# Kernel tuning notes

Hardware: AMD Instinct MI355X
Metric: run time of the kernel (lower is better)

The kernel has to match this reference:

```python
import jax, jax.numpy as jnp
import numpy as np

N_HEAD = 16
D_MODEL = 1024
D_HEAD = D_MODEL // N_HEAD  # 64
B, S = 1, 4096


def setup_inputs() -> dict:
    key = jax.random.key(0)
    ks = jax.random.split(key, 7)
    q = jax.random.normal(ks[0], (B, S, D_MODEL), dtype=jnp.float32)
    k = jax.random.normal(ks[1], (B, S, D_MODEL), dtype=jnp.float32)
    v = jax.random.normal(ks[2], (B, S, D_MODEL), dtype=jnp.float32)
    mask = jnp.ones((S, S), dtype=bool)
    # params match torch.rand init (uniform [0,1)); use uniform here too
    w_q = jax.random.uniform(ks[3], (D_MODEL, D_MODEL), dtype=jnp.float32)
    w_k = jax.random.uniform(ks[4], (D_HEAD, D_MODEL), dtype=jnp.float32)
    w_v = jax.random.uniform(ks[5], (D_HEAD, D_MODEL), dtype=jnp.float32)
    w_out = jax.random.uniform(ks[6], (D_MODEL, D_MODEL), dtype=jnp.float32)
    return {"q": q, "k": k, "v": v, "mask": mask,
            "w_q": w_q, "w_k": w_k, "w_v": w_v, "w_out": w_out}


def reference(q, k, v, mask, w_q, w_k, w_v, w_out):
    # F.linear(x, W) == x @ W.T
    query = q @ w_q.T                      # [b, n, d_model]
    key = k @ w_k.T                        # [b, s, d_head]  (single shared KV head)
    value = v @ w_v.T                      # [b, s, d_head]
    b, n, _ = query.shape
    query = query.reshape(b, n, N_HEAD, D_HEAD).transpose(0, 2, 1, 3)  # b h n d
    scores = jnp.einsum('bhnd,bsd->bhns', query, key) / jnp.sqrt(jnp.float32(D_HEAD))
    scores = jnp.where(mask[None, None], scores, jnp.float32(-jnp.inf))
    attn = jax.nn.softmax(scores, axis=-1)             # [b, h, n, s]
    out = jnp.einsum('bhns,bsd->bhnd', attn, value)    # [b, h, n, d]
    out = out.transpose(0, 2, 1, 3).reshape(b, n, D_MODEL)
    return out @ w_out.T
```

## Files before the change

kernel.cpp:

```cpp
#include <hip/hip_runtime.h>
#include <cstdint>
#include <cstddef>

#define S_LEN   4096
#define DM      1024
#define NHEAD   16
#define DH      64

typedef short bf16x8 __attribute__((ext_vector_type(8)));
typedef _Float16 f16x8 __attribute__((ext_vector_type(8)));
typedef float f32x4  __attribute__((ext_vector_type(4)));

__device__ __forceinline__ unsigned short f2bf(float x) {
    uint32_t u = __float_as_uint(x);
    u += 0x7fffu + ((u >> 16) & 1u);
    return (unsigned short)(u >> 16);
}
__device__ __forceinline__ float bf2f(unsigned short u) {
    return __uint_as_float(((uint32_t)u) << 16);
}
__device__ __forceinline__ unsigned pack_bf2(float a, float b) {
    return (unsigned)f2bf(a) | ((unsigned)f2bf(b) << 16);
}
__device__ __forceinline__ unsigned short f2h(float x) {
    _Float16 h = (_Float16)x;
    return __builtin_bit_cast(unsigned short, h);
}
__device__ __forceinline__ unsigned pack_h2(float a, float b) {
    return __builtin_bit_cast(unsigned, __builtin_amdgcn_cvt_pkrtz(a, b));
}
__device__ __forceinline__ void gl_lds16(const unsigned short* g, unsigned short* l) {
    __builtin_amdgcn_global_load_lds(
        (const __attribute__((address_space(1))) unsigned int*)g,
        (__attribute__((address_space(3))) unsigned int*)l, 16, 0, 0);
}
__device__ __forceinline__ void split8(const float4& a0, const float4& a1,
                                       ushort4& h0, ushort4& h1,
                                       ushort4& l0, ushort4& l1) {
    h0.x = f2bf(a0.x); l0.x = f2bf(a0.x - bf2f(h0.x));
    h0.y = f2bf(a0.y); l0.y = f2bf(a0.y - bf2f(h0.y));
    h0.z = f2bf(a0.z); l0.z = f2bf(a0.z - bf2f(h0.z));
    h0.w = f2bf(a0.w); l0.w = f2bf(a0.w - bf2f(h0.w));
    h1.x = f2bf(a1.x); l1.x = f2bf(a1.x - bf2f(h1.x));
    h1.y = f2bf(a1.y); l1.y = f2bf(a1.y - bf2f(h1.y));
    h1.z = f2bf(a1.z); l1.z = f2bf(a1.z - bf2f(h1.z));
    h1.w = f2bf(a1.w); l1.w = f2bf(a1.w - bf2f(h1.w));
}

__global__ void cvt_qw(const float* __restrict__ q, const float* __restrict__ wq,
                       const float* __restrict__ wo,
                       unsigned short* __restrict__ qh, unsigned short* __restrict__ ql,
                       unsigned short* __restrict__ wqh, unsigned short* __restrict__ wql,
                       unsigned short* __restrict__ woh)
{
    const int G1 = 1048576, GW = 262144;
    int i = blockIdx.x * blockDim.x + threadIdx.x;
    const float* src; unsigned short* h; unsigned short* l = nullptr; int off;
    if (i < G1)            { src = q;  h = qh;  l = ql;  off = i; }
    else if (i < G1 + GW)  { src = wq; h = wqh; l = wql; off = i - G1; }
    else                   { src = wo; h = woh;          off = i - G1 - GW; }
    float4 vv = reinterpret_cast<const float4*>(src)[off];
    ushort4 hh;
    hh.x = f2bf(vv.x); hh.y = f2bf(vv.y); hh.z = f2bf(vv.z); hh.w = f2bf(vv.w);
    reinterpret_cast<ushort4*>(h)[off] = hh;
    if (l) {
        ushort4 ll;
        ll.x = f2bf(vv.x - bf2f(hh.x)); ll.y = f2bf(vv.y - bf2f(hh.y));
        ll.z = f2bf(vv.z - bf2f(hh.z)); ll.w = f2bf(vv.w - bf2f(hh.w));
        reinterpret_cast<ushort4*>(l)[off] = ll;
    }
}

__launch_bounds__(256)
__global__ void kv_proj(const float* __restrict__ kin, const float* __restrict__ vin,
                        const float* __restrict__ wk, const float* __restrict__ wv,
                        unsigned short* __restrict__ Kf, unsigned short* __restrict__ Vtf)
{
    __shared__ unsigned short As_h[64][72];
    __shared__ unsigned short Bs_h[64][72];
    __shared__ unsigned short As_l[64][72];
    __shared__ unsigned short Bs_l[64][72];

    const int tid  = threadIdx.x;
    const int wave = tid >> 6;
    const int lane = tid & 63;
    const int lm   = lane & 15;
    const int quad = lane >> 4;
    const int m0   = blockIdx.x * 64;
    const bool isK = (blockIdx.y == 0);
    const float* A = isK ? kin : vin;
    const float* B = isK ? wk : wv;

    f32x4 acc[4] = {};

    for (int kc = 0; kc < DM; kc += 64) {
        __syncthreads();
#pragma unroll
        for (int i = 0; i < 2; ++i) {
            int c   = tid + i * 256;
            int r   = c >> 3;
            int col = (c & 7) * 8;
            float4 a0 = *(const float4*)&A[(size_t)(m0 + r) * DM + kc + col];
            float4 a1 = *(const float4*)&A[(size_t)(m0 + r) * DM + kc + col + 4];
            float4 b0 = *(const float4*)&B[(size_t)r * DM + kc + col];
            float4 b1 = *(const float4*)&B[(size_t)r * DM + kc + col + 4];
            ushort4 h0, h1, l0, l1;
            split8(a0, a1, h0, h1, l0, l1);
            *(ushort4*)&As_h[r][col] = h0;  *(ushort4*)&As_h[r][col + 4] = h1;
            if (isK) { *(ushort4*)&As_l[r][col] = l0;  *(ushort4*)&As_l[r][col + 4] = l1; }
            split8(b0, b1, h0, h1, l0, l1);
            *(ushort4*)&Bs_h[r][col] = h0;  *(ushort4*)&Bs_h[r][col + 4] = h1;
            if (isK) { *(ushort4*)&Bs_l[r][col] = l0;  *(ushort4*)&Bs_l[r][col + 4] = l1; }
        }
        __syncthreads();
#pragma unroll
        for (int kk = 0; kk < 64; kk += 32) {
            bf16x8 bh = *(const bf16x8*)&Bs_h[wave * 16 + lm][kk + quad * 8];
            bf16x8 bl;
            if (isK) bl = *(const bf16x8*)&Bs_l[wave * 16 + lm][kk + quad * 8];
#pragma unroll
            for (int ms = 0; ms < 4; ++ms) {
                bf16x8 ah = *(const bf16x8*)&As_h[ms * 16 + lm][kk + quad * 8];
                acc[ms] = __builtin_amdgcn_mfma_f32_16x16x32_bf16(ah, bh, acc[ms], 0, 0, 0);
                if (isK) {
                    bf16x8 al = *(const bf16x8*)&As_l[ms * 16 + lm][kk + quad * 8];
                    acc[ms] = __builtin_amdgcn_mfma_f32_16x16x32_bf16(ah, bl, acc[ms], 0, 0, 0);
                    acc[ms] = __builtin_amdgcn_mfma_f32_16x16x32_bf16(al, bh, acc[ms], 0, 0, 0);
                }
            }
        }
    }

#pragma unroll
    for (int ms = 0; ms < 4; ++ms)
#pragma unroll
        for (int r = 0; r < 4; ++r) {
            int row = m0 + ms * 16 + quad * 4 + r;
            int col = wave * 16 + lm;
            if (isK) Kf[(size_t)row * DH + col] = f2h(acc[ms][r]);
            else     Vtf[(size_t)col * S_LEN + row] = f2h(acc[ms][r]);
        }
}

__launch_bounds__(256)
__global__ void gemm_big(const unsigned short* __restrict__ Ah,
                         const unsigned short* __restrict__ Al,
                         const unsigned short* __restrict__ Bh,
                         const unsigned short* __restrict__ Bl,
                         unsigned short* __restrict__ Ch,
                         int M, int N, int K, int ldc)
{
    __shared__ unsigned short As_h[2][8192];
    __shared__ unsigned short Bs_h[2][8192];
    __shared__ unsigned short As_l[2][8192];
    __shared__ unsigned short Bs_l[2][8192];

    const int tid  = threadIdx.x;
    const int wave = tid >> 6;
    const int lane = tid & 63;
    const int lm   = lane & 15;
    const int quad = lane >> 4;
    const int wm   = wave >> 1;
    const int wn   = wave & 1;
    const int m0   = blockIdx.x * 128;
    const int n0   = blockIdx.y * 128;

    int srow[4], scol[4];
#pragma unroll
    for (int i = 0; i < 4; ++i) {
        int f = i * 256 + tid;
        srow[i] = f >> 3;
        scol[i] = ((f & 7) ^ (srow[i] & 7)) * 8;
    }

    auto stage = [&](int b, int kc) {
#pragma unroll
        for (int i = 0; i < 4; ++i) {
            const int dst = (i * 256 + wave * 64) * 8;
            gl_lds16(&Ah[(size_t)(m0 + srow[i]) * K + kc + scol[i]], &As_h[b][dst]);
            gl_lds16(&Bh[(size_t)(n0 + srow[i]) * K + kc + scol[i]], &Bs_h[b][dst]);
            gl_lds16(&Al[(size_t)(m0 + srow[i]) * K + kc + scol[i]], &As_l[b][dst]);
            gl_lds16(&Bl[(size_t)(n0 + srow[i]) * K + kc + scol[i]], &Bs_l[b][dst]);
        }
    };

    stage(0, 0);

    f32x4 acc[4][4] = {};
    const int nkc = K / 64;

    for (int it = 0; it < nkc; ++it) {
        const int b = it & 1;
        __syncthreads();
        if (it + 1 < nkc) stage(b ^ 1, (it + 1) * 64);

#pragma unroll
        for (int kk = 0; kk < 2; ++kk) {
            bf16x8 bh[4], bl[4];
#pragma unroll
            for (int ns = 0; ns < 4; ++ns) {
                const int off = (wn * 64 + ns * 16 + lm) * 64 + ((kk * 4 + quad) ^ (lm & 7)) * 8;
                bh[ns] = *(const bf16x8*)&Bs_h[b][off];
                bl[ns] = *(const bf16x8*)&Bs_l[b][off];
            }
#pragma unroll
            for (int ms = 0; ms < 4; ++ms) {
                const int off = (wm * 64 + ms * 16 + lm) * 64 + ((kk * 4 + quad) ^ (lm & 7)) * 8;
                bf16x8 ah = *(const bf16x8*)&As_h[b][off];
                bf16x8 al = *(const bf16x8*)&As_l[b][off];
#pragma unroll
                for (int ns = 0; ns < 4; ++ns) {
                    acc[ms][ns] = __builtin_amdgcn_mfma_f32_16x16x32_bf16(ah, bh[ns], acc[ms][ns], 0, 0, 0);
                    acc[ms][ns] = __builtin_amdgcn_mfma_f32_16x16x32_bf16(ah, bl[ns], acc[ms][ns], 0, 0, 0);
                    acc[ms][ns] = __builtin_amdgcn_mfma_f32_16x16x32_bf16(al, bh[ns], acc[ms][ns], 0, 0, 0);
                }
            }
        }
    }

#pragma unroll
    for (int ms = 0; ms < 4; ++ms)
#pragma unroll
        for (int ns = 0; ns < 4; ++ns)
#pragma unroll
            for (int r = 0; r < 4; ++r) {
                int row = m0 + wm * 64 + ms * 16 + quad * 4 + r;
                int col = n0 + wn * 64 + ns * 16 + lm;
                Ch[(size_t)row * ldc + col] = f2h(acc[ms][ns][r]);
            }
}

__launch_bounds__(256)
__global__ void flash_kernel(const unsigned short* __restrict__ Qf,
                             const unsigned short* __restrict__ Kf,
                             const unsigned short* __restrict__ Vt,
                             unsigned short* __restrict__ Op,
                             float* __restrict__ Mb,
                             float* __restrict__ Lb)
{
    __shared__ unsigned short Ks[2][4096];
    __shared__ unsigned short Vs[2][4096];

    const int tid  = threadIdx.x;
    const int wave = tid >> 6;
    const int lane = tid & 63;
    const int lm   = lane & 15;
    const int quad = lane >> 4;
    const int q0   = blockIdx.x * 128;
    const int h    = blockIdx.y;
    const int sp   = blockIdx.z;
    const int kbase = sp * (S_LEN / 2);
    const float c  = 0.125f * 1.44269504f;

    const int r0 = tid >> 3,         c0 = ((tid & 7) ^ (r0 & 7)) * 8;
    const int r1 = (tid + 256) >> 3, c1 = ((tid & 7) ^ (r1 & 7)) * 8;
    const int ldsA = wave * 512;
    const int ldsB = 2048 + wave * 512;

    auto stage = [&](int kt, int b) {
        gl_lds16(&Kf[(size_t)(kt + r0) * DH + c0], &Ks[b][ldsA]);
        gl_lds16(&Kf[(size_t)(kt + r1) * DH + c1], &Ks[b][ldsB]);
        gl_lds16(&Vt[(size_t)r0 * S_LEN + kt + c0], &Vs[b][ldsA]);
        gl_lds16(&Vt[(size_t)r1 * S_LEN + kt + c1], &Vs[b][ldsB]);
    };

    stage(kbase, 0);

    f16x8 qf[2][2];
#pragma unroll
    for (int nb = 0; nb < 2; ++nb)
#pragma unroll
        for (int kk = 0; kk < 2; ++kk) {
            size_t idx = (size_t)(q0 + wave * 32 + nb * 16 + lm) * DM + h * DH + kk * 32 + quad * 8;
            qf[nb][kk] = *(const f16x8*)&Qf[idx];
        }

    f32x4 oacc[2][4] = {};
    float m_run[2] = {-1e30f, -1e30f}, l_run[2] = {0.f, 0.f};

    for (int it = 0; it < 32; ++it) {
        const int b = it & 1;
        const int kt = kbase + it * 64;
        __syncthreads();
        if (it + 1 < 32) stage(kt + 64, b ^ 1);

        f32x4 sacc[2][4] = {};
#pragma unroll
        for (int kk = 0; kk < 2; ++kk) {
#pragma unroll
            for (int ms = 0; ms < 4; ++ms) {
                const int off = (ms * 16 + lm) * 64 + ((4 * kk + quad) ^ (lm & 7)) * 8;
                f16x8 kfr = *(const f16x8*)&Ks[b][off];
#pragma unroll
                for (int nb = 0; nb < 2; ++nb)
                    sacc[nb][ms] = __builtin_amdgcn_mfma_f32_16x16x32_f16(kfr, qf[nb][kk], sacc[nb][ms], 0, 0, 0);
            }
        }

        float mn[2];
#pragma unroll
        for (int nb = 0; nb < 2; ++nb) {
            float mx = -1e30f;
#pragma unroll
            for (int ms = 0; ms < 4; ++ms)
#pragma unroll
                for (int r = 0; r < 4; ++r) mx = fmaxf(mx, sacc[nb][ms][r]);
            mx = fmaxf(mx, __shfl_xor(mx, 16));
            mx = fmaxf(mx, __shfl_xor(mx, 32));
            mn[nb] = fmaxf(m_run[nb], mx);
        }

        if (__any((mn[0] > m_run[0]) || (mn[1] > m_run[1]))) {
#pragma unroll
            for (int mq = 0; mq < 2; ++mq) {
                float alpha = __builtin_amdgcn_exp2f((m_run[mq] - mn[mq]) * c);
                l_run[mq] *= alpha;
                m_run[mq] = mn[mq];
                float ar[4];
#pragma unroll
                for (int r = 0; r < 4; ++r) ar[r] = __shfl(alpha, quad * 4 + r);
#pragma unroll
                for (int nd = 0; nd < 4; ++nd)
#pragma unroll
                    for (int r = 0; r < 4; ++r) oacc[mq][nd][r] *= ar[r];
            }
        }

        unsigned pk[2][4][2];
#pragma unroll
        for (int nb = 0; nb < 2; ++nb) {
            float mc = m_run[nb] * c;
            float ps = 0.f;
#pragma unroll
            for (int ms = 0; ms < 4; ++ms) {
                float pr[4];
#pragma unroll
                for (int r = 0; r < 4; ++r) {
                    pr[r] = __builtin_amdgcn_exp2f(fmaf(sacc[nb][ms][r], c, -mc));
                    ps += pr[r];
                }
                pk[nb][ms][0] = pack_h2(pr[0], pr[1]);
                pk[nb][ms][1] = pack_h2(pr[2], pr[3]);
            }
            ps += __shfl_xor(ps, 16);
            ps += __shfl_xor(ps, 32);
            l_run[nb] += ps;
        }

#pragma unroll
        for (int kb = 0; kb < 2; ++kb) {
            f16x8 pa[2];
#pragma unroll
            for (int nb = 0; nb < 2; ++nb) {
                unsigned af[4] __attribute__((aligned(16)));
#pragma unroll
                for (int d = 0; d < 4; ++d) {
                    int srcl = ((2 * quad + (d >> 1)) & 3) * 16 + lm;
                    unsigned v_lo = (unsigned)__shfl((int)pk[nb][2 * kb][d & 1], srcl);
                    unsigned v_hi = (unsigned)__shfl((int)pk[nb][2 * kb + 1][d & 1], srcl);
                    af[d] = (quad < 2) ? v_lo : v_hi;
                }
                pa[nb] = *(f16x8*)af;
            }
#pragma unroll
            for (int nd = 0; nd < 4; ++nd) {
                const int off = (nd * 16 + lm) * 64 + ((4 * kb + quad) ^ (lm & 7)) * 8;
                f16x8 vb = *(const f16x8*)&Vs[b][off];
#pragma unroll
                for (int nb = 0; nb < 2; ++nb)
                    oacc[nb][nd] = __builtin_amdgcn_mfma_f32_16x16x32_f16(pa[nb], vb, oacc[nb][nd], 0, 0, 0);
            }
        }
    }

    unsigned short* Osp = Op + (size_t)sp * NHEAD * S_LEN * DH;
#pragma unroll
    for (int mq = 0; mq < 2; ++mq) {
#pragma unroll
        for (int nd = 0; nd < 4; ++nd)
#pragma unroll
            for (int r = 0; r < 4; ++r) {
                int q = q0 + wave * 32 + mq * 16 + quad * 4 + r;
                Osp[((size_t)h * S_LEN + q) * DH + nd * 16 + lm] = f2bf(oacc[mq][nd][r]);
            }
        if (quad == 0) {
            int q = q0 + wave * 32 + mq * 16 + lm;
            Mb[(size_t)sp * NHEAD * S_LEN + h * S_LEN + q] = m_run[mq];
            Lb[(size_t)sp * NHEAD * S_LEN + h * S_LEN + q] = l_run[mq];
        }
    }
}

__launch_bounds__(256)
__global__ void out_proj(const unsigned short* __restrict__ Op,
                         const float* __restrict__ Mb,
                         const float* __restrict__ Lb,
                         const unsigned short* __restrict__ Wo,
                         float* __restrict__ out)
{
    __shared__ unsigned short As[64][72];
    __shared__ unsigned short Bs[64][72];

    const int tid  = threadIdx.x;
    const int wave = tid >> 6;
    const int lane = tid & 63;
    const int lm   = lane & 15;
    const int quad = lane >> 4;
    const int m0   = blockIdx.x * 64;
    const int n0   = blockIdx.y * 64;
    const float c  = 0.125f * 1.44269504f;
    const int HS   = NHEAD * S_LEN;
    const size_t OSP = (size_t)NHEAD * S_LEN * DH;

    f32x4 acc[4] = {};

    for (int it = 0; it < 16; ++it) {
        __syncthreads();
#pragma unroll
        for (int i = 0; i < 2; ++i) {
            int cc  = tid + i * 256;
            int r   = cc >> 3;
            int col = (cc & 7) * 8;
            int q   = m0 + r;
            int hq  = it * S_LEN + q;
            float m1 = Mb[hq], m2 = Mb[HS + hq];
            float l1 = Lb[hq], l2 = Lb[HS + hq];
            float mm = fmaxf(m1, m2);
            float w1 = __builtin_amdgcn_exp2f((m1 - mm) * c);
            float w2 = __builtin_amdgcn_exp2f((m2 - mm) * c);
            float inv = 1.0f / (l1 * w1 + l2 * w2);
            w1 *= inv; w2 *= inv;
            size_t base = ((size_t)it * S_LEN + q) * DH + col;
            uint4 u1 = *(const uint4*)&Op[base];
            uint4 u2 = *(const uint4*)&Op[OSP + base];
            unsigned mrg[4];
            const unsigned* p1 = (const unsigned*)&u1;
            const unsigned* p2 = (const unsigned*)&u2;
#pragma unroll
            for (int d = 0; d < 4; ++d) {
                float a = bf2f((unsigned short)(p1[d] & 0xffff)) * w1
                        + bf2f((unsigned short)(p2[d] & 0xffff)) * w2;
                float b = bf2f((unsigned short)(p1[d] >> 16)) * w1
                        + bf2f((unsigned short)(p2[d] >> 16)) * w2;
                mrg[d] = pack_bf2(a, b);
            }
            *(uint4*)&As[r][col] = *(uint4*)mrg;
            *(uint4*)&Bs[r][col] = *(const uint4*)&Wo[(size_t)(n0 + r) * DM + it * 64 + col];
        }
        __syncthreads();
#pragma unroll
        for (int kk = 0; kk < 64; kk += 32) {
            bf16x8 bh = *(const bf16x8*)&Bs[wave * 16 + lm][kk + quad * 8];
#pragma unroll
            for (int ms = 0; ms < 4; ++ms) {
                bf16x8 ah = *(const bf16x8*)&As[ms * 16 + lm][kk + quad * 8];
                acc[ms] = __builtin_amdgcn_mfma_f32_16x16x32_bf16(ah, bh, acc[ms], 0, 0, 0);
            }
        }
    }

#pragma unroll
    for (int ms = 0; ms < 4; ++ms)
#pragma unroll
        for (int r = 0; r < 4; ++r) {
            int row = m0 + ms * 16 + quad * 4 + r;
            int col = n0 + wave * 16 + lm;
            out[(size_t)row * DM + col] = acc[ms][r];
        }
}

extern "C" void kernel_launch(void* const* d_in, const int* in_sizes, int n_in,
                              void* d_out, int out_size, void* d_ws, size_t ws_size,
                              hipStream_t stream)
{
    (void)in_sizes; (void)n_in; (void)out_size; (void)ws_size;
    const float* q     = (const float*)d_in[0];
    const float* k     = (const float*)d_in[1];
    const float* v     = (const float*)d_in[2];
    const float* w_q   = (const float*)d_in[4];
    const float* w_k   = (const float*)d_in[5];
    const float* w_v   = (const float*)d_in[6];
    const float* w_out = (const float*)d_in[7];
    float* out = (float*)d_out;

    char* ws = (char*)d_ws;
    size_t off = 0;
    auto alloc = [&](size_t bytes) -> unsigned short* {
        unsigned short* p = (unsigned short*)(ws + off);
        off += (bytes + 255) & ~(size_t)255;
        return p;
    };
    const size_t SZ_QKV = (size_t)S_LEN * DM * 2;
    const size_t SZ_WQ  = (size_t)DM * DM * 2;
    const size_t SZ_KV  = (size_t)S_LEN * DH * 2;

    unsigned short* qh  = alloc(SZ_QKV);
    unsigned short* ql  = alloc(SZ_QKV);
    unsigned short* wqh = alloc(SZ_WQ);
    unsigned short* wql = alloc(SZ_WQ);
    unsigned short* woh = alloc(SZ_WQ);
    unsigned short* Qf  = alloc(SZ_QKV);
    unsigned short* Kf  = alloc(SZ_KV);
    unsigned short* Vtf = alloc(SZ_KV);
    unsigned short* Op  = alloc(2 * NHEAD * SZ_KV);
    float* Mb = (float*)alloc(2 * NHEAD * S_LEN * 4);
    float* Lb = (float*)alloc(2 * NHEAD * S_LEN * 4);

    kv_proj<<<dim3(64, 2), 256, 0, stream>>>(k, v, w_k, w_v, Kf, Vtf);

    cvt_qw<<<dim3(6144), 256, 0, stream>>>(q, w_q, w_out, qh, ql, wqh, wql, woh);

    gemm_big<<<dim3(32, 8), 256, 0, stream>>>(qh, ql, wqh, wql, Qf, S_LEN, DM, DM, DM);

    flash_kernel<<<dim3(32, 16, 2), 256, 0, stream>>>(Qf, Kf, Vtf, Op, Mb, Lb);

    out_proj<<<dim3(64, 16), 256, 0, stream>>>(Op, Mb, Lb, woh, out);
}
```

Measured before the change: 376.8 us.

## Merge KV projection with conversion, split flash-attention four ways, widen out_proj tile

Merges the K/V projection and the fp32-to-bf16 conversion kernels into one launch, selected by block index. This removes a launch and lets the small kv_proj grid overlap with the conversion blocks. Raises the flash-attention KV split count from 2 to 4, doubling the grid to 2048 blocks for better CU occupancy at the cost of more partial-output traffic. The out_proj tile is widened to 128 columns, halving the redundant split-merge work per output, though it now reads four partials.

```diff
diff --git a/kernel.cpp b/kernel.cpp
--- a/kernel.cpp
+++ b/kernel.cpp
@@ -6,6 +6,7 @@
 #define DM      1024
 #define NHEAD   16
 #define DH      64
+#define SPLITS  4
 
 typedef short bf16x8 __attribute__((ext_vector_type(8)));
 typedef _Float16 f16x8 __attribute__((ext_vector_type(8)));
@@ -47,47 +48,50 @@
     h1.w = f2bf(a1.w); l1.w = f2bf(a1.w - bf2f(h1.w));
 }
 
-__global__ void cvt_qw(const float* __restrict__ q, const float* __restrict__ wq,
-                       const float* __restrict__ wo,
-                       unsigned short* __restrict__ qh, unsigned short* __restrict__ ql,
-                       unsigned short* __restrict__ wqh, unsigned short* __restrict__ wql,
-                       unsigned short* __restrict__ woh)
-{
-    const int G1 = 1048576, GW = 262144;
-    int i = blockIdx.x * blockDim.x + threadIdx.x;
-    const float* src; unsigned short* h; unsigned short* l = nullptr; int off;
-    if (i < G1)            { src = q;  h = qh;  l = ql;  off = i; }
-    else if (i < G1 + GW)  { src = wq; h = wqh; l = wql; off = i - G1; }
-    else                   { src = wo; h = woh;          off = i - G1 - GW; }
-    float4 vv = reinterpret_cast<const float4*>(src)[off];
-    ushort4 hh;
-    hh.x = f2bf(vv.x); hh.y = f2bf(vv.y); hh.z = f2bf(vv.z); hh.w = f2bf(vv.w);
-    reinterpret_cast<ushort4*>(h)[off] = hh;
-    if (l) {
-        ushort4 ll;
-        ll.x = f2bf(vv.x - bf2f(hh.x)); ll.y = f2bf(vv.y - bf2f(hh.y));
-        ll.z = f2bf(vv.z - bf2f(hh.z)); ll.w = f2bf(vv.w - bf2f(hh.w));
-        reinterpret_cast<ushort4*>(l)[off] = ll;
-    }
-}
-
 __launch_bounds__(256)
-__global__ void kv_proj(const float* __restrict__ kin, const float* __restrict__ vin,
-                        const float* __restrict__ wk, const float* __restrict__ wv,
-                        unsigned short* __restrict__ Kf, unsigned short* __restrict__ Vtf)
+__global__ void pre_kernel(const float* __restrict__ kin, const float* __restrict__ vin,
+                           const float* __restrict__ wk, const float* __restrict__ wv,
+                           const float* __restrict__ q, const float* __restrict__ wq,
+                           const float* __restrict__ wo,
+                           unsigned short* __restrict__ Kf, unsigned short* __restrict__ Vtf,
+                           unsigned short* __restrict__ qh, unsigned short* __restrict__ ql,
+                           unsigned short* __restrict__ wqh, unsigned short* __restrict__ wql,
+                           unsigned short* __restrict__ woh)
 {
     __shared__ unsigned short As_h[64][72];
     __shared__ unsigned short Bs_h[64][72];
     __shared__ unsigned short As_l[64][72];
     __shared__ unsigned short Bs_l[64][72];
 
-    const int tid  = threadIdx.x;
+    const int tid = threadIdx.x;
+    const int bx  = blockIdx.x;
+
+    if (bx >= 128) {
+        const int G1 = 1048576, GW = 262144;
+        int i = (bx - 128) * 256 + tid;
+        const float* src; unsigned short* h; unsigned short* l = nullptr; int off;
+        if (i < G1)            { src = q;  h = qh;  l = ql;  off = i; }
+        else if (i < G1 + GW)  { src = wq; h = wqh; l = wql; off = i - G1; }
+        else                   { src = wo; h = woh;          off = i - G1 - GW; }
+        float4 vv = reinterpret_cast<const float4*>(src)[off];
+        ushort4 hh;
+        hh.x = f2bf(vv.x); hh.y = f2bf(vv.y); hh.z = f2bf(vv.z); hh.w = f2bf(vv.w);
+        reinterpret_cast<ushort4*>(h)[off] = hh;
+        if (l) {
+            ushort4 ll;
+            ll.x = f2bf(vv.x - bf2f(hh.x)); ll.y = f2bf(vv.y - bf2f(hh.y));
+            ll.z = f2bf(vv.z - bf2f(hh.z)); ll.w = f2bf(vv.w - bf2f(hh.w));
+            reinterpret_cast<ushort4*>(l)[off] = ll;
+        }
+        return;
+    }
+
     const int wave = tid >> 6;
     const int lane = tid & 63;
     const int lm   = lane & 15;
     const int quad = lane >> 4;
-    const int m0   = blockIdx.x * 64;
-    const bool isK = (blockIdx.y == 0);
+    const bool isK = (bx < 64);
+    const int m0   = (bx & 63) * 64;
     const float* A = isK ? kin : vin;
     const float* B = isK ? wk : wv;
 
@@ -249,7 +253,8 @@
     const int q0   = blockIdx.x * 128;
     const int h    = blockIdx.y;
     const int sp   = blockIdx.z;
-    const int kbase = sp * (S_LEN / 2);
+    const int kbase = sp * (S_LEN / SPLITS);
+    const int NIT  = S_LEN / SPLITS / 64;
     const float c  = 0.125f * 1.44269504f;
 
     const int r0 = tid >> 3,         c0 = ((tid & 7) ^ (r0 & 7)) * 8;
@@ -278,11 +283,11 @@
     f32x4 oacc[2][4] = {};
     float m_run[2] = {-1e30f, -1e30f}, l_run[2] = {0.f, 0.f};
 
-    for (int it = 0; it < 32; ++it) {
+    for (int it = 0; it < NIT; ++it) {
         const int b = it & 1;
         const int kt = kbase + it * 64;
         __syncthreads();
-        if (it + 1 < 32) stage(kt + 64, b ^ 1);
+        if (it + 1 < NIT) stage(kt + 64, b ^ 1);
 
         f32x4 sacc[2][4] = {};
 #pragma unroll
@@ -399,7 +404,7 @@
                          float* __restrict__ out)
 {
     __shared__ unsigned short As[64][72];
-    __shared__ unsigned short Bs[64][72];
+    __shared__ unsigned short Bs[128][72];
 
     const int tid  = threadIdx.x;
     const int wave = tid >> 6;
@@ -407,12 +412,12 @@
     const int lm   = lane & 15;
     const int quad = lane >> 4;
     const int m0   = blockIdx.x * 64;
-    const int n0   = blockIdx.y * 64;
+    const int n0   = blockIdx.y * 128;
     const float c  = 0.125f * 1.44269504f;
     const int HS   = NHEAD * S_LEN;
     const size_t OSP = (size_t)NHEAD * S_LEN * DH;
 
-    f32x4 acc[4] = {};
+    f32x4 acc[4][2] = {};
 
     for (int it = 0; it < 16; ++it) {
         __syncthreads();
@@ -423,38 +428,62 @@
             int col = (cc & 7) * 8;
             int q   = m0 + r;
             int hq  = it * S_LEN + q;
-            float m1 = Mb[hq], m2 = Mb[HS + hq];
-            float l1 = Lb[hq], l2 = Lb[HS + hq];
-            float mm = fmaxf(m1, m2);
-            float w1 = __builtin_amdgcn_exp2f((m1 - mm) * c);
-            float w2 = __builtin_amdgcn_exp2f((m2 - mm) * c);
-            float inv = 1.0f / (l1 * w1 + l2 * w2);
-            w1 *= inv; w2 *= inv;
+            float m_i[SPLITS], l_i[SPLITS];
+            float mm = -1e30f;
+#pragma unroll
+            for (int s = 0; s < SPLITS; ++s) {
+                m_i[s] = Mb[s * HS + hq];
+                l_i[s] = Lb[s * HS + hq];
+                mm = fmaxf(mm, m_i[s]);
+            }
+            float w_i[SPLITS], denom = 0.f;
+#pragma unroll
+            for (int s = 0; s < SPLITS; ++s) {
+                w_i[s] = __builtin_amdgcn_exp2f((m_i[s] - mm) * c);
+                denom += l_i[s] * w_i[s];
+            }
+            float inv = 1.0f / denom;
+#pragma unroll
+            for (int s = 0; s < SPLITS; ++s) w_i[s] *= inv;
+
             size_t base = ((size_t)it * S_LEN + q) * DH + col;
-            uint4 u1 = *(const uint4*)&Op[base];
-            uint4 u2 = *(const uint4*)&Op[OSP + base];
+            uint4 u[SPLITS];
+#pragma unroll
+            for (int s = 0; s < SPLITS; ++s) u[s] = *(const uint4*)&Op[s * OSP + base];
             unsigned mrg[4];
-            const unsigned* p1 = (const unsigned*)&u1;
-            const unsigned* p2 = (const unsigned*)&u2;
 #pragma unroll
             for (int d = 0; d < 4; ++d) {
-                float a = bf2f((unsigned short)(p1[d] & 0xffff)) * w1
-                        + bf2f((unsigned short)(p2[d] & 0xffff)) * w2;
-                float b = bf2f((unsigned short)(p1[d] >> 16)) * w1
-                        + bf2f((unsigned short)(p2[d] >> 16)) * w2;
+                float a = 0.f, b = 0.f;
+#pragma unroll
+                for (int s = 0; s < SPLITS; ++s) {
+                    unsigned uu = ((const unsigned*)&u[s])[d];
+                    a = fmaf(bf2f((unsigned short)(uu & 0xffff)), w_i[s], a);
+                    b = fmaf(bf2f((unsigned short)(uu >> 16)),    w_i[s], b);
+                }
                 mrg[d] = pack_bf2(a, b);
             }
             *(uint4*)&As[r][col] = *(uint4*)mrg;
+        }
+#pragma unroll
+        for (int i = 0; i < 4; ++i) {
+            int cc  = tid + i * 256;
+            int r   = cc >> 3;
+            int col = (cc & 7) * 8;
             *(uint4*)&Bs[r][col] = *(const uint4*)&Wo[(size_t)(n0 + r) * DM + it * 64 + col];
         }
         __syncthreads();
 #pragma unroll
         for (int kk = 0; kk < 64; kk += 32) {
-            bf16x8 bh = *(const bf16x8*)&Bs[wave * 16 + lm][kk + quad * 8];
+            bf16x8 bh[2];
+#pragma unroll
+            for (int ns = 0; ns < 2; ++ns)
+                bh[ns] = *(const bf16x8*)&Bs[wave * 32 + ns * 16 + lm][kk + quad * 8];
 #pragma unroll
             for (int ms = 0; ms < 4; ++ms) {
                 bf16x8 ah = *(const bf16x8*)&As[ms * 16 + lm][kk + quad * 8];
-                acc[ms] = __builtin_amdgcn_mfma_f32_16x16x32_bf16(ah, bh, acc[ms], 0, 0, 0);
+#pragma unroll
+                for (int ns = 0; ns < 2; ++ns)
+                    acc[ms][ns] = __builtin_amdgcn_mfma_f32_16x16x32_bf16(ah, bh[ns], acc[ms][ns], 0, 0, 0);
             }
         }
     }
@@ -462,11 +491,13 @@
 #pragma unroll
     for (int ms = 0; ms < 4; ++ms)
 #pragma unroll
-        for (int r = 0; r < 4; ++r) {
-            int row = m0 + ms * 16 + quad * 4 + r;
-            int col = n0 + wave * 16 + lm;
-            out[(size_t)row * DM + col] = acc[ms][r];
-        }
+        for (int ns = 0; ns < 2; ++ns)
+#pragma unroll
+            for (int r = 0; r < 4; ++r) {
+                int row = m0 + ms * 16 + quad * 4 + r;
+                int col = n0 + wave * 32 + ns * 16 + lm;
+                out[(size_t)row * DM + col] = acc[ms][ns][r];
+            }
 }
 
 extern "C" void kernel_launch(void* const* d_in, const int* in_sizes, int n_in,
@@ -502,17 +533,16 @@
     unsigned short* Qf  = alloc(SZ_QKV);
     unsigned short* Kf  = alloc(SZ_KV);
     unsigned short* Vtf = alloc(SZ_KV);
-    unsigned short* Op  = alloc(2 * NHEAD * SZ_KV);
-    float* Mb = (float*)alloc(2 * NHEAD * S_LEN * 4);
-    float* Lb = (float*)alloc(2 * NHEAD * S_LEN * 4);
-
-    kv_proj<<<dim3(64, 2), 256, 0, stream>>>(k, v, w_k, w_v, Kf, Vtf);
-
-    cvt_qw<<<dim3(6144), 256, 0, stream>>>(q, w_q, w_out, qh, ql, wqh, wql, woh);
+    unsigned short* Op  = alloc(SPLITS * NHEAD * SZ_KV);
+    float* Mb = (float*)alloc(SPLITS * NHEAD * S_LEN * 4);
+    float* Lb = (float*)alloc(SPLITS * NHEAD * S_LEN * 4);
+
+    pre_kernel<<<dim3(6272), 256, 0, stream>>>(k, v, w_k, w_v, q, w_q, w_out,
+                                               Kf, Vtf, qh, ql, wqh, wql, woh);
 
     gemm_big<<<dim3(32, 8), 256, 0, stream>>>(qh, ql, wqh, wql, Qf, S_LEN, DM, DM, DM);
 
-    flash_kernel<<<dim3(32, 16, 2), 256, 0, stream>>>(Qf, Kf, Vtf, Op, Mb, Lb);
-
-    out_proj<<<dim3(64, 16), 256, 0, stream>>>(Op, Mb, Lb, woh, out);
-}
+    flash_kernel<<<dim3(32, 16, SPLITS), 256, 0, stream>>>(Qf, Kf, Vtf, Op, Mb, Lb);
+
+    out_proj<<<dim3(64, 8), 256, 0, stream>>>(Op, Mb, Lb, woh, out);
+}
```

Result: slower. 397.7 us (+5.6%).
